# Optimization experiments

Measured on AMD Instinct MI355X. Metric: run time of the kernel, lower is better.

Reference implementation:

```python
import jax, jax.numpy as jnp
import numpy as np

CAT_CARDS = [10, 20, 15, 8, 30, 12, 5, 25, 6, 40, 18, 9]   # categorical_card entries with card > 1 (first 20 entries)
NUM = 32          # num_numerical
NBIN = 8          # categorical_card[:-2] entries with card == 1
NLIKE = 2         # last two categorical_card entries, both card 1
NMASK = NUM + len(CAT_CARDS) + NBIN + NLIKE   # 32 + 22 = 54 mask heads
LAT, HID, B = 128, 1024, 16384
TAU = 1.0
EPS = 1e-20


def setup_inputs() -> dict:
    key = jax.random.key(0)
    ks = jax.random.split(key, 7)
    w = lambda k, sh: (jax.random.normal(k, sh, jnp.float32) * 0.02)
    return {
        "z": jax.random.normal(ks[0], (B, LAT), jnp.float32),
        "W1": w(ks[1], (LAT, HID)), "b1": jnp.zeros((HID,), jnp.float32),
        "W_num": w(ks[2], (HID, NUM)), "b_num": jnp.zeros((NUM,), jnp.float32),
        "W_cat": w(ks[3], (HID, sum(CAT_CARDS))), "b_cat": jnp.zeros((sum(CAT_CARDS),), jnp.float32),
        "W_bin": w(ks[4], (HID, NBIN)), "b_bin": jnp.zeros((NBIN,), jnp.float32),
        "W_like": w(ks[5], (HID, NLIKE)), "b_like": jnp.zeros((NLIKE,), jnp.float32),
        "W_mask": w(ks[6], (HID, NMASK)), "b_mask": jnp.zeros((NMASK,), jnp.float32),
    }


def _gumbel_sigmoid(logits, key, tau=TAU):
    # matches torch: noise~U(0,1); g = -log(-log(noise+eps)+eps); sigmoid((logits+g)/tau); hard=False
    u = jax.random.uniform(key, logits.shape, logits.dtype)
    g = -jnp.log(-jnp.log(u + EPS) + EPS)
    return jax.nn.sigmoid((logits + g) / tau)


def reference(z, W1, b1, W_num, b_num, W_cat, b_cat, W_bin, b_bin, W_like, b_like, W_mask, b_mask):
    nk = jax.random.split(jax.random.key(1), 3)
    h = jax.nn.relu(z @ W1 + b1)                       # [B, HID]
    num_out = h @ W_num + b_num                        # [B, NUM]

    cat_logits = h @ W_cat + b_cat                     # [B, sum(cards)] fused GEMM, then split per head
    splits = np.cumsum(CAT_CARDS)[:-1].tolist()
    cat_out = tuple(jnp.split(cat_logits, splits, axis=1))

    # use_gumbel=True, hard=False: binary / likewise / mask heads get gumbel-sigmoid
    bin_out = _gumbel_sigmoid(h @ W_bin + b_bin, nk[0])      # [B, NBIN]
    like_out = _gumbel_sigmoid(h @ W_like + b_like, nk[1])   # [B, NLIKE]
    mask_out = _gumbel_sigmoid(h @ W_mask + b_mask, nk[2])   # [B, NMASK]

    bins = tuple(bin_out[:, i:i + 1] for i in range(NBIN))
    likes = tuple(like_out[:, i:i + 1] for i in range(NLIKE))
    masks = tuple(mask_out[:, i:i + 1] for i in range(NMASK))
    return (num_out,) + cat_out + bins + likes + masks
```

## Files before the change

kernel.cpp:

```cpp
#include <hip/hip_runtime.h>
#include <stdint.h>

#define B_ROWS 16384
#define LATD   128
#define HIDD   1024

typedef __bf16 bf16x8 __attribute__((ext_vector_type(8)));
typedef float  f32x4  __attribute__((ext_vector_type(4)));
typedef float  f32x4v __attribute__((ext_vector_type(4)));
typedef unsigned short ushort8v __attribute__((ext_vector_type(8)));
typedef unsigned int   uint2v   __attribute__((ext_vector_type(2)));

template<int N> __device__ __forceinline__ void waitv() {
  asm volatile("s_waitcnt vmcnt(%0)" :: "i"(N) : "memory");
  __builtin_amdgcn_sched_barrier(0);
}
__device__ __forceinline__ void gl16(bf16x8& r, const unsigned short* p) {
  asm volatile("global_load_dwordx4 %0, %1, off" : "=v"(r) : "v"(p));
}
template<int OFF> __device__ __forceinline__ void gl16o(bf16x8& r, const unsigned short* p) {
  asm volatile("global_load_dwordx4 %0, %1, off offset:%2" : "=v"(r) : "v"(p), "i"(OFF));
}
#define LGKM_BARRIER() do {                                        \
    asm volatile("s_waitcnt lgkmcnt(0)" ::: "memory");             \
    __builtin_amdgcn_s_barrier();                                  \
    asm volatile("" ::: "memory");                                 \
  } while (0)

struct TF2 { unsigned int a, b; };

#define TF_R(x0,x1,r) { x0 += x1; x1 = ((x1 << (r)) | (x1 >> (32 - (r)))); x1 ^= x0; }

__host__ __device__ constexpr TF2 threefry2x32(unsigned k0, unsigned k1, unsigned c0, unsigned c1) {
  unsigned ks2 = k0 ^ k1 ^ 0x1BD11BDAu;
  unsigned x0 = c0 + k0, x1 = c1 + k1;
  TF_R(x0,x1,13) TF_R(x0,x1,15) TF_R(x0,x1,26) TF_R(x0,x1,6)
  x0 += k1;  x1 += ks2 + 1u;
  TF_R(x0,x1,17) TF_R(x0,x1,29) TF_R(x0,x1,16) TF_R(x0,x1,24)
  x0 += ks2; x1 += k0 + 2u;
  TF_R(x0,x1,13) TF_R(x0,x1,15) TF_R(x0,x1,26) TF_R(x0,x1,6)
  x0 += k0;  x1 += k1 + 3u;
  TF_R(x0,x1,17) TF_R(x0,x1,29) TF_R(x0,x1,16) TF_R(x0,x1,24)
  x0 += k1;  x1 += ks2 + 4u;
  TF_R(x0,x1,13) TF_R(x0,x1,15) TF_R(x0,x1,26) TF_R(x0,x1,6)
  x0 += ks2; x1 += k0 + 5u;
  return {x0, x1};
}

constexpr TF2 NK0 = threefry2x32(0u, 1u, 0u, 0u);
constexpr TF2 NK1 = threefry2x32(0u, 1u, 0u, 1u);
constexpr TF2 NK2 = threefry2x32(0u, 1u, 0u, 2u);

__device__ __forceinline__ unsigned short f2bf(float f) {
  unsigned u = __float_as_uint(f);
  return (unsigned short)((u + 0x7fffu + ((u >> 16) & 1u)) >> 16);
}

__global__ void prep_kernel(const float* __restrict__ W1,
                            const float* __restrict__ Wnum, const float* __restrict__ Wcat,
                            const float* __restrict__ Wbin, const float* __restrict__ Wlike,
                            const float* __restrict__ Wmask,
                            const float* __restrict__ bnum, const float* __restrict__ bcat,
                            const float* __restrict__ bbin, const float* __restrict__ blike,
                            const float* __restrict__ bmask,
                            unsigned short* __restrict__ W1p,
                            unsigned short* __restrict__ Wallp,
                            float* __restrict__ ball) {
  int t = blockIdx.x * 256 + threadIdx.x;
  if (t < 16384) {
    int f = t >> 6, l = t & 63;
    int n = (f >> 2) * 16 + (l & 15);
    int kk0 = (f & 3) * 32 + (l >> 4) * 8;
    ushort8v p;
    #pragma unroll
    for (int j = 0; j < 8; ++j) p[j] = f2bf(W1[(size_t)(kk0 + j) * HIDD + n]);
    *(ushort8v*)(W1p + (size_t)t * 8) = p;
  } else if (t < 16384 + 40960) {
    int t2 = t - 16384;
    int g = t2 >> 6, l = t2 & 63;
    int nt = g >> 5, kt = g & 31;
    int n = nt * 16 + (l & 15);
    int kk0 = kt * 32 + (l >> 4) * 8;
    ushort8v p;
    #pragma unroll
    for (int j = 0; j < 8; ++j) {
      int kk = kk0 + j;
      float v = 0.f;
      if (n < 32)       v = Wnum [(size_t)kk * 32  + n];
      else if (n < 230) v = Wcat [(size_t)kk * 198 + (n - 32)];
      else if (n < 238) v = Wbin [(size_t)kk * 8   + (n - 230)];
      else if (n < 240) v = Wlike[(size_t)kk * 2   + (n - 238)];
      else if (n < 294) v = Wmask[(size_t)kk * 54  + (n - 240)];
      p[j] = f2bf(v);
    }
    *(ushort8v*)(Wallp + (size_t)t2 * 8) = p;
  } else if (t < 16384 + 40960 + 320) {
    int n = t - (16384 + 40960);
    float v = 0.f;
    if (n < 32)       v = bnum [n];
    else if (n < 230) v = bcat [n - 32];
    else if (n < 238) v = bbin [n - 230];
    else if (n < 240) v = blike[n - 238];
    else if (n < 294) v = bmask[n - 240];
    ball[n] = v;
  }
}

template<int G>
__device__ __forceinline__ void run_phases(
    const int w, const int lane, const int l15, const int l4, const int nt0,
    const unsigned short* __restrict__ W1p, const unsigned short* __restrict__ Wallp,
    const float* __restrict__ b1,
    unsigned char* smem, f32x4 (&acc)[4][3]) {

  unsigned short* zs = (unsigned short*)smem;
  unsigned char* hbase  = smem + 17408;
  unsigned char* mytile = hbase + w * 16384;

  f32x4 hb1[8];
  #pragma unroll
  for (int ct = 0; ct < 8; ++ct)
    hb1[ct] = *(const f32x4*)(b1 + w * 128 + ct * 16 + l4 * 4);

  bf16x8 za[4][4];
  #pragma unroll
  for (int rt = 0; rt < 4; ++rt)
    #pragma unroll
    for (int ks = 0; ks < 4; ++ks)
      za[rt][ks] = *(const bf16x8*)(zs + (rt * 16 + l15) * 136 + ks * 32 + l4 * 8);

  bf16x8 wq1[2][4];
  const unsigned short* w1b = W1p + (size_t)w * 16384 + lane * 8;
  #pragma unroll
  for (int ct = 0; ct < 2; ++ct) {
    const unsigned short* p = w1b + ct * 2048;
    gl16o<0>(wq1[ct][0], p); gl16o<1024>(wq1[ct][1], p);
    gl16o<2048>(wq1[ct][2], p); gl16o<3072>(wq1[ct][3], p);
  }

  bf16x8 wq2[4][G];
  const unsigned short* w2b = Wallp + lane * 8;

  #pragma unroll
  for (int ct = 0; ct < 8; ++ct) {
    if (ct < 7) waitv<4>();
    else        waitv<G * 4>();
    f32x4 a[4] = {};
    #pragma unroll
    for (int ks = 0; ks < 4; ++ks)
      #pragma unroll
      for (int rt = 0; rt < 4; ++rt)
        a[rt] = __builtin_amdgcn_mfma_f32_16x16x32_bf16(wq1[ct & 1][ks], za[rt][ks], a[rt], 0, 0, 0);
    #pragma unroll
    for (int rt = 0; rt < 4; ++rt) {
      float v0 = fmaxf(a[rt][0] + hb1[ct][0], 0.f);
      float v1 = fmaxf(a[rt][1] + hb1[ct][1], 0.f);
      float v2 = fmaxf(a[rt][2] + hb1[ct][2], 0.f);
      float v3 = fmaxf(a[rt][3] + hb1[ct][3], 0.f);
      uint2v u;
      u[0] = (unsigned)f2bf(v0) | ((unsigned)f2bf(v1) << 16);
      u[1] = (unsigned)f2bf(v2) | ((unsigned)f2bf(v3) << 16);
      const int byte = ((ct >> 1) * 4 + rt) * 1024
                     + ((ct & 1) * 2 + (l4 >> 1)) * 256
                     + l15 * 16 + (l4 & 1) * 8;
      *(uint2v*)(mytile + byte) = u;
    }
    if (ct < 6) {
      const unsigned short* p = w1b + (ct + 2) * 2048;
      gl16o<0>(wq1[ct & 1][0], p); gl16o<1024>(wq1[ct & 1][1], p);
      gl16o<2048>(wq1[ct & 1][2], p); gl16o<3072>(wq1[ct & 1][3], p);
    } else if (ct == 6) {
      #pragma unroll
      for (int g = 0; g < 4; ++g)
        #pragma unroll
        for (int cc = 0; cc < G; ++cc)
          gl16(wq2[g][cc], w2b + (size_t)((nt0 + cc) * 32 + g) * 512);
    }
  }

  LGKM_BARRIER();

  #pragma unroll
  for (int rt = 0; rt < 4; ++rt)
    #pragma unroll
    for (int ct = 0; ct < 3; ++ct)
      acc[rt][ct] = (f32x4){0.f, 0.f, 0.f, 0.f};

  #pragma unroll
  for (int g = 0; g < 32; ++g) {
    if (g < 29)      waitv<G * 3>();
    else if (g == 29) waitv<G * 2>();
    else if (g == 30) waitv<G>();
    else              waitv<0>();
    const unsigned char* hc = hbase + (g >> 2) * 16384 + (g & 3) * 4096 + lane * 16;
    #pragma unroll
    for (int rt = 0; rt < 4; ++rt) {
      bf16x8 ha = *(const bf16x8*)(hc + rt * 1024);
      #pragma unroll
      for (int ct = 0; ct < G; ++ct)
        acc[rt][ct] = __builtin_amdgcn_mfma_f32_16x16x32_bf16(ha, wq2[g & 3][ct], acc[rt][ct], 0, 0, 0);
    }
    if (g + 4 < 32) {
      #pragma unroll
      for (int cc = 0; cc < G; ++cc)
        gl16(wq2[g & 3][cc], w2b + (size_t)((nt0 + cc) * 32 + (g + 4)) * 512);
    }
  }
}

__global__ __launch_bounds__(512, 2) void decoder_kernel(
    const float* __restrict__ z, const float* __restrict__ b1,
    const unsigned short* __restrict__ W1p, const unsigned short* __restrict__ Wallp,
    const float* __restrict__ ball, float* __restrict__ out) {
  __shared__ __align__(16) unsigned char smem[148480];
  unsigned short* zs = (unsigned short*)smem;
  float* outs = (float*)smem;

  const int tid  = threadIdx.x;
  const int lane = tid & 63;
  const int w    = tid >> 6;
  const int l15  = lane & 15;
  const int l4   = lane >> 4;
  const int r0   = blockIdx.x * 64;

  #pragma unroll
  for (int it = 0; it < 2; ++it) {
    int ch  = tid + it * 512;
    int row = ch >> 4;
    int k0  = (ch & 15) * 8;
    const float* src = z + (size_t)(r0 + row) * LATD + k0;
    f32x4v f0 = __builtin_nontemporal_load((const f32x4v*)src);
    f32x4v f1 = __builtin_nontemporal_load((const f32x4v*)(src + 4));
    ushort8v p;
    p[0] = f2bf(f0[0]); p[1] = f2bf(f0[1]); p[2] = f2bf(f0[2]); p[3] = f2bf(f0[3]);
    p[4] = f2bf(f1[0]); p[5] = f2bf(f1[1]); p[6] = f2bf(f1[2]); p[7] = f2bf(f1[3]);
    *(ushort8v*)(zs + row * 136 + k0) = p;
  }
  __syncthreads();

  const int cb  = (w < 4) ? w * 48 : 192 + (w - 4) * 32;
  const int nt0 = (w < 4) ? w * 3  : 12 + (w - 4) * 2;
  const int myG = (w < 4) ? 3 : 2;

  f32x4 acc[4][3];
  if (w < 4) run_phases<3>(w, lane, l15, l4, nt0, W1p, Wallp, b1, smem, acc);
  else       run_phases<2>(w, lane, l15, l4, nt0, W1p, Wallp, b1, smem, acc);

  __syncthreads();

  #pragma unroll
  for (int ct = 0; ct < 3; ++ct) {
    if (ct < myG) {
      float b2 = ball[cb + ct * 16 + l15];
      #pragma unroll
      for (int rt = 0; rt < 4; ++rt)
        #pragma unroll
        for (int j = 0; j < 4; ++j)
          outs[(rt * 16 + l4 * 4 + j) * 321 + cb + ct * 16 + l15] = acc[rt][ct][j] + b2;
    }
  }
  __syncthreads();

  {
    constexpr int cards[13] = {32,10,20,15,8,30,12,5,25,6,40,18,9};
    constexpr int cbase[13] = {0,32,42,62,77,85,115,127,132,157,163,203,221};
    #pragma unroll
    for (int blk = 0; blk < 13; ++blk) {
      const int card = cards[blk];
      const int cbs  = cbase[blk];
      float* gout = out + (size_t)B_ROWS * cbs + (size_t)r0 * card;
      for (int v = tid; v < card * 16; v += 512) {
        int gg = v * 4;
        f32x4v vbuf;
        #pragma unroll
        for (int e = 0; e < 4; ++e) {
          int ge = gg + e;
          int brow = ge / card;
          int j = ge - brow * card;
          vbuf[e] = outs[brow * 321 + cbs + j];
        }
        __builtin_nontemporal_store(vbuf, (f32x4v*)(gout + gg));
      }
    }
  }

  {
    int c = 230 + (tid >> 3);
    unsigned ka, kb; int Nh, head;
    if (c < 238)      { ka = NK0.a; kb = NK0.b; Nh = 8;  head = c - 230; }
    else if (c < 240) { ka = NK1.a; kb = NK1.b; Nh = 2;  head = c - 238; }
    else              { ka = NK2.a; kb = NK2.b; Nh = 54; head = c - 240; }
    #pragma unroll
    for (int q = 0; q < 2; ++q) {
      int rq = (tid & 7) * 4 + q * 32;
      f32x4v vbuf;
      #pragma unroll
      for (int e = 0; e < 4; ++e) {
        int rl = rq + e;
        float x = outs[rl * 321 + c];
        unsigned j = (unsigned)((r0 + rl) * Nh + head);
        TF2 t = threefry2x32(ka, kb, 0u, j);
        unsigned bits = t.a ^ t.b;
        float u  = __uint_as_float((bits >> 9) | 0x3f800000u) - 1.0f;
        float gn = -logf(-logf(u + 1e-20f) + 1e-20f);
        vbuf[e] = 1.0f / (1.0f + expf(-(x + gn)));
      }
      __builtin_nontemporal_store(vbuf, (f32x4v*)(out + (size_t)B_ROWS * c + r0 + rq));
    }
  }
}

extern "C" void kernel_launch(void* const* d_in, const int* in_sizes, int n_in,
                              void* d_out, int out_size, void* d_ws, size_t ws_size,
                              hipStream_t stream) {
  const float* z     = (const float*)d_in[0];
  const float* W1    = (const float*)d_in[1];
  const float* b1    = (const float*)d_in[2];
  const float* Wnum  = (const float*)d_in[3];
  const float* bnum  = (const float*)d_in[4];
  const float* Wcat  = (const float*)d_in[5];
  const float* bcat  = (const float*)d_in[6];
  const float* Wbin  = (const float*)d_in[7];
  const float* bbin  = (const float*)d_in[8];
  const float* Wlike = (const float*)d_in[9];
  const float* blike = (const float*)d_in[10];
  const float* Wmask = (const float*)d_in[11];
  const float* bmask = (const float*)d_in[12];

  unsigned short* W1p   = (unsigned short*)d_ws;
  unsigned short* Wallp = W1p + 131072;
  float*          ball  = (float*)(Wallp + 327680);

  const int total = 16384 + 40960 + 320;
  prep_kernel<<<(total + 255) / 256, 256, 0, stream>>>(
      W1, Wnum, Wcat, Wbin, Wlike, Wmask, bnum, bcat, bbin, blike, bmask,
      W1p, Wallp, ball);

  decoder_kernel<<<B_ROWS / 64, 512, 0, stream>>>(
      z, b1, W1p, Wallp, ball, (float*)d_out);
}
```

Before: 29.50 us.

## Transpose weights through LDS in prep, raise MFMA wave priority, use fast math

The weight-prep kernel now stages tiles in shared memory, so W1 reads are coalesced float4 loads and the packed bf16 fragments go out as contiguous 16-byte stores. The old version did strided scalar gathers. The grid shrinks to 97 blocks. The decoder wraps its MFMA loops in s_setprio to favor matrix issue, and the gumbel-sigmoid epilogue swaps logf/expf for the fast __logf/__expf intrinsics, which are slightly less accurate.

```diff
diff --git a/kernel.cpp b/kernel.cpp
--- a/kernel.cpp
+++ b/kernel.cpp
@@ -56,53 +56,79 @@
   return (unsigned short)((u + 0x7fffu + ((u >> 16) & 1u)) >> 16);
 }
 
-__global__ void prep_kernel(const float* __restrict__ W1,
-                            const float* __restrict__ Wnum, const float* __restrict__ Wcat,
-                            const float* __restrict__ Wbin, const float* __restrict__ Wlike,
-                            const float* __restrict__ Wmask,
-                            const float* __restrict__ bnum, const float* __restrict__ bcat,
-                            const float* __restrict__ bbin, const float* __restrict__ blike,
-                            const float* __restrict__ bmask,
-                            unsigned short* __restrict__ W1p,
-                            unsigned short* __restrict__ Wallp,
-                            float* __restrict__ ball) {
-  int t = blockIdx.x * 256 + threadIdx.x;
-  if (t < 16384) {
-    int f = t >> 6, l = t & 63;
-    int n = (f >> 2) * 16 + (l & 15);
-    int kk0 = (f & 3) * 32 + (l >> 4) * 8;
-    ushort8v p;
-    #pragma unroll
-    for (int j = 0; j < 8; ++j) p[j] = f2bf(W1[(size_t)(kk0 + j) * HIDD + n]);
-    *(ushort8v*)(W1p + (size_t)t * 8) = p;
-  } else if (t < 16384 + 40960) {
-    int t2 = t - 16384;
-    int g = t2 >> 6, l = t2 & 63;
-    int nt = g >> 5, kt = g & 31;
-    int n = nt * 16 + (l & 15);
-    int kk0 = kt * 32 + (l >> 4) * 8;
-    ushort8v p;
-    #pragma unroll
-    for (int j = 0; j < 8; ++j) {
-      int kk = kk0 + j;
+__global__ __launch_bounds__(256) void prep_kernel(
+    const float* __restrict__ W1,
+    const float* __restrict__ Wnum, const float* __restrict__ Wcat,
+    const float* __restrict__ Wbin, const float* __restrict__ Wlike,
+    const float* __restrict__ Wmask,
+    const float* __restrict__ bnum, const float* __restrict__ bcat,
+    const float* __restrict__ bbin, const float* __restrict__ blike,
+    const float* __restrict__ bmask,
+    unsigned short* __restrict__ W1p,
+    unsigned short* __restrict__ Wallp,
+    float* __restrict__ ball) {
+  __shared__ __align__(16) unsigned short lds[8704];
+  const int b = blockIdx.x, t = threadIdx.x;
+
+  if (b < 16) {
+    const int n0 = b * 64;
+    #pragma unroll
+    for (int i = 0; i < 8; ++i) {
+      int linear = i * 256 + t;
+      int k = linear >> 4, nq = linear & 15;
+      f32x4 v = *(const f32x4*)(W1 + (size_t)k * HIDD + n0 + nq * 4);
+      #pragma unroll
+      for (int e = 0; e < 4; ++e) lds[(nq * 4 + e) * 136 + k] = f2bf(v[e]);
+    }
+    __syncthreads();
+    #pragma unroll
+    for (int i = 0; i < 4; ++i) {
+      int linear = i * 256 + t;
+      int f_loc = linear >> 6, l = linear & 63;
+      int l15 = l & 15, l4 = l >> 4;
+      int n_loc = (f_loc >> 2) * 16 + l15;
+      int k = (f_loc & 3) * 32 + l4 * 8;
+      ushort8v p = *(const ushort8v*)(lds + n_loc * 136 + k);
+      *(ushort8v*)(W1p + ((size_t)(b * 16 + f_loc) * 64 + l) * 8) = p;
+    }
+  } else if (b < 96) {
+    const int q  = b - 16;
+    const int nt = q >> 2, ktb = q & 3;
+    const int n0 = nt * 16, k0 = ktb * 256;
+    const int n = n0 + (t & 15);
+    #pragma unroll
+    for (int i = 0; i < 16; ++i) {
+      int kk_loc = i * 16 + (t >> 4);
+      int kk = k0 + kk_loc;
       float v = 0.f;
       if (n < 32)       v = Wnum [(size_t)kk * 32  + n];
       else if (n < 230) v = Wcat [(size_t)kk * 198 + (n - 32)];
       else if (n < 238) v = Wbin [(size_t)kk * 8   + (n - 230)];
       else if (n < 240) v = Wlike[(size_t)kk * 2   + (n - 238)];
       else if (n < 294) v = Wmask[(size_t)kk * 54  + (n - 240)];
-      p[j] = f2bf(v);
-    }
-    *(ushort8v*)(Wallp + (size_t)t2 * 8) = p;
-  } else if (t < 16384 + 40960 + 320) {
-    int n = t - (16384 + 40960);
-    float v = 0.f;
-    if (n < 32)       v = bnum [n];
-    else if (n < 230) v = bcat [n - 32];
-    else if (n < 238) v = bbin [n - 230];
-    else if (n < 240) v = blike[n - 238];
-    else if (n < 294) v = bmask[n - 240];
-    ball[n] = v;
+      lds[(t & 15) * 264 + kk_loc] = f2bf(v);
+    }
+    __syncthreads();
+    #pragma unroll
+    for (int i = 0; i < 2; ++i) {
+      int linear = i * 256 + t;
+      int kt_loc = linear >> 6, l = linear & 63;
+      int l15 = l & 15, l4 = l >> 4;
+      int koff = kt_loc * 32 + l4 * 8;
+      ushort8v p = *(const ushort8v*)(lds + l15 * 264 + koff);
+      int g = nt * 32 + ktb * 8 + kt_loc;
+      *(ushort8v*)(Wallp + ((size_t)g * 64 + l) * 8) = p;
+    }
+  } else {
+    for (int n = t; n < 320; n += 256) {
+      float v = 0.f;
+      if (n < 32)       v = bnum [n];
+      else if (n < 230) v = bcat [n - 32];
+      else if (n < 238) v = bbin [n - 230];
+      else if (n < 240) v = blike[n - 238];
+      else if (n < 294) v = bmask[n - 240];
+      ball[n] = v;
+    }
   }
 }
 
@@ -146,11 +172,13 @@
     if (ct < 7) waitv<4>();
     else        waitv<G * 4>();
     f32x4 a[4] = {};
+    __builtin_amdgcn_s_setprio(1);
     #pragma unroll
     for (int ks = 0; ks < 4; ++ks)
       #pragma unroll
       for (int rt = 0; rt < 4; ++rt)
         a[rt] = __builtin_amdgcn_mfma_f32_16x16x32_bf16(wq1[ct & 1][ks], za[rt][ks], a[rt], 0, 0, 0);
+    __builtin_amdgcn_s_setprio(0);
     #pragma unroll
     for (int rt = 0; rt < 4; ++rt) {
       float v0 = fmaxf(a[rt][0] + hb1[ct][0], 0.f);
@@ -188,11 +216,12 @@
 
   #pragma unroll
   for (int g = 0; g < 32; ++g) {
-    if (g < 29)      waitv<G * 3>();
+    if (g < 29)       waitv<G * 3>();
     else if (g == 29) waitv<G * 2>();
     else if (g == 30) waitv<G>();
     else              waitv<0>();
     const unsigned char* hc = hbase + (g >> 2) * 16384 + (g & 3) * 4096 + lane * 16;
+    __builtin_amdgcn_s_setprio(1);
     #pragma unroll
     for (int rt = 0; rt < 4; ++rt) {
       bf16x8 ha = *(const bf16x8*)(hc + rt * 1024);
@@ -200,6 +229,7 @@
       for (int ct = 0; ct < G; ++ct)
         acc[rt][ct] = __builtin_amdgcn_mfma_f32_16x16x32_bf16(ha, wq2[g & 3][ct], acc[rt][ct], 0, 0, 0);
     }
+    __builtin_amdgcn_s_setprio(0);
     if (g + 4 < 32) {
       #pragma unroll
       for (int cc = 0; cc < G; ++cc)
@@ -302,8 +332,8 @@
         TF2 t = threefry2x32(ka, kb, 0u, j);
         unsigned bits = t.a ^ t.b;
         float u  = __uint_as_float((bits >> 9) | 0x3f800000u) - 1.0f;
-        float gn = -logf(-logf(u + 1e-20f) + 1e-20f);
-        vbuf[e] = 1.0f / (1.0f + expf(-(x + gn)));
+        float gn = -__logf(-__logf(u + 1e-20f) + 1e-20f);
+        vbuf[e] = 1.0f / (1.0f + __expf(-(x + gn)));
       }
       __builtin_nontemporal_store(vbuf, (f32x4v*)(out + (size_t)B_ROWS * c + r0 + rq));
     }
@@ -331,8 +361,7 @@
   unsigned short* Wallp = W1p + 131072;
   float*          ball  = (float*)(Wallp + 327680);
 
-  const int total = 16384 + 40960 + 320;
-  prep_kernel<<<(total + 255) / 256, 256, 0, stream>>>(
+  prep_kernel<<<97, 256, 0, stream>>>(
       W1, Wnum, Wcat, Wbin, Wlike, Wmask, bnum, bcat, bbin, blike, bmask,
       W1p, Wallp, ball);
 
```

Result: slower. 30.24 us (+2.5%).
